# Performance work log

Hardware: AMD Instinct MI355X
Metric: run time of the kernel (lower is better)

Reference implementation:

```python
import jax, jax.numpy as jnp
import numpy as np

B, L, DIM, H, D = 2, 2048, 1024, 16, 64


def setup_inputs() -> dict:
    key = jax.random.key(0)
    ks = jax.random.split(key, 20)
    s = 1.0 / np.sqrt(DIM)
    inp = {
        "query": jax.random.normal(ks[0], (B, L, DIM), jnp.float32),
        "keys": jax.random.normal(ks[1], (B, L, DIM), jnp.float32),
        "values": jax.random.normal(ks[2], (B, L, DIM), jnp.float32),
        "focus_vector": jax.random.normal(ks[3], (B, DIM), jnp.float32),
        "temporal_weights": jax.random.normal(ks[4], (B, L), jnp.float32),
        "importance_weights": jax.random.normal(ks[5], (B, L), jnp.float32),
        # linear params, stored [in, out] for x @ W + b
        "Wq": jax.random.normal(ks[6], (DIM, H * D), jnp.float32) * s,
        "bq": jnp.zeros((H * D,), jnp.float32),
        "Wk": jax.random.normal(ks[7], (DIM, H * D), jnp.float32) * s,
        "bk": jnp.zeros((H * D,), jnp.float32),
        "Wv": jax.random.normal(ks[8], (DIM, H * D), jnp.float32) * s,
        "bv": jnp.zeros((H * D,), jnp.float32),
        "Wp": jax.random.normal(ks[9], (H * D, DIM), jnp.float32) * s,
        "bp": jnp.zeros((DIM,), jnp.float32),
        "Wt": jax.random.normal(ks[10], (DIM, 1), jnp.float32) * s,
        "bt": jnp.zeros((1,), jnp.float32),
        "Wi": jax.random.normal(ks[11], (DIM, 1), jnp.float32) * s,
        "bi": jnp.zeros((1,), jnp.float32),
    }
    return inp


def reference(query, keys, values, focus_vector, temporal_weights, importance_weights,
              Wq, bq, Wk, bk, Wv, bv, Wp, bp, Wt, bt, Wi, bi):
    b, l, _ = query.shape
    # QKV projections -> [B, H, L, D]
    q = (query @ Wq + bq).reshape(b, l, H, D).transpose(0, 2, 1, 3)
    k = (keys @ Wk + bk).reshape(b, -1, H, D).transpose(0, 2, 1, 3)
    v = (values @ Wv + bv).reshape(b, -1, H, D).transpose(0, 2, 1, 3)
    scores = jnp.einsum("bhqd,bhkd->bhqk", q, k) / np.sqrt(D).astype(np.float32)
    # gate-modulated weights over keys [B, Lk]
    temporal_scores = (keys @ Wt + bt)[..., 0]
    tw = jax.nn.softmax(temporal_scores * temporal_weights, axis=-1)
    importance_scores = (keys @ Wi + bi)[..., 0]
    iw = jax.nn.softmax(importance_scores * importance_weights, axis=-1)
    rw = jax.nn.softmax(jnp.einsum("bkd,bd->bk", keys, focus_vector), axis=-1)
    combined = (tw + iw + rw) / 3.0
    scores = scores * combined[:, None, None, :]
    weights = jax.nn.softmax(scores, axis=-1)  # dropout is identity in eval
    out = jnp.einsum("bhqk,bhkd->bhqd", weights, v)
    out = out.transpose(0, 2, 1, 3).reshape(b, l, H * D)
    out = out @ Wp + bp
    return out, weights
```

## Files before the change

kernel.cpp:

```cpp
#include <hip/hip_runtime.h>
#include <hip/hip_bf16.h>
#include <cstdint>

#define DEV static __device__ __forceinline__

typedef __attribute__((ext_vector_type(8))) short short8_;
typedef __attribute__((ext_vector_type(4))) float float4_;
typedef __attribute__((ext_vector_type(4))) float f4v;
typedef __attribute__((ext_vector_type(4))) unsigned short u16x4;
typedef unsigned short u16;

constexpr int Bb   = 2;
constexpr int Ls   = 2048;
constexpr int DIMc = 1024;
constexpr int Hh   = 16;
constexpr int Dd   = 64;
constexpr int BL   = Bb * Ls;
constexpr int HD   = Hh * Dd;

DEV u16 f2bf(float f) {
  union { float f; uint32_t u; } v; v.f = f;
  return (u16)((v.u + 0x7fffu + ((v.u >> 16) & 1u)) >> 16);
}

DEV float4_ mfma16(short8_ a, short8_ b, float4_ c) {
  return __builtin_amdgcn_mfma_f32_16x16x32_bf16(a, b, c, 0, 0, 0);
}

DEV void gload_lds16(const void* g, void* l) {
  __builtin_amdgcn_global_load_lds(
      (const __attribute__((address_space(1))) void*)g,
      (__attribute__((address_space(3))) void*)l, 16, 0, 0);
}

__global__ void k_cast3(const float* __restrict__ a, const float* __restrict__ b,
                        const float* __restrict__ c, u16* __restrict__ oa,
                        u16* __restrict__ ob, u16* __restrict__ oc) {
  int z = blockIdx.y;
  const float* s = (z == 0) ? a : (z == 1) ? b : c;
  u16* d = (z == 0) ? oa : (z == 1) ? ob : oc;
  int i = blockIdx.x * 256 + threadIdx.x;
  f4v v = ((const f4v*)s)[i];
  u16x4 o = { f2bf(v[0]), f2bf(v[1]), f2bf(v[2]), f2bf(v[3]) };
  ((u16x4*)d)[i] = o;
}

__global__ void k_trans4(const float* __restrict__ W0, const float* __restrict__ W1,
                         const float* __restrict__ W2, const float* __restrict__ W3,
                         u16* __restrict__ T0, u16* __restrict__ T1,
                         u16* __restrict__ T2, u16* __restrict__ T3) {
  __shared__ float t[64][65];
  int z = blockIdx.z;
  const float* W = (z == 0) ? W0 : (z == 1) ? W1 : (z == 2) ? W2 : W3;
  u16* WT = (z == 0) ? T0 : (z == 1) ? T1 : (z == 2) ? T2 : T3;
  int tx = threadIdx.x & 63;
  int tg = threadIdx.x >> 6;
  int n0 = blockIdx.x * 64;
  int k0 = blockIdx.y * 64;
#pragma unroll
  for (int i = 0; i < 16; ++i) {
    int r = tg * 16 + i;
    t[r][tx] = W[(size_t)(k0 + r) * HD + n0 + tx];
  }
  __syncthreads();
#pragma unroll
  for (int i = 0; i < 16; ++i) {
    int r = tg * 16 + i;
    WT[(size_t)(n0 + r) * DIMc + k0 + tx] = f2bf(t[tx][r]);
  }
}

__global__ void k_gates(const float* __restrict__ keys, const float* __restrict__ Wt,
                        const float* __restrict__ bt, const float* __restrict__ Wi,
                        const float* __restrict__ bi, const float* __restrict__ focus,
                        float* __restrict__ ts, float* __restrict__ is_, float* __restrict__ rs) {
  int wv = threadIdx.x >> 6, ln = threadIdx.x & 63;
  int row = blockIdx.x * 4 + wv;
  int b = row >> 11;
  const float* kr = keys + (size_t)row * DIMc;
  const float* fr = focus + (size_t)b * DIMc;
  float st = 0.f, si = 0.f, sr = 0.f;
  for (int j = ln; j < DIMc; j += 64) {
    float kv = kr[j];
    st += kv * Wt[j]; si += kv * Wi[j]; sr += kv * fr[j];
  }
#pragma unroll
  for (int m = 1; m < 64; m <<= 1) {
    st += __shfl_xor(st, m); si += __shfl_xor(si, m); sr += __shfl_xor(sr, m);
  }
  if (ln == 0) { ts[row] = st + bt[0]; is_[row] = si + bi[0]; rs[row] = sr; }
}

__global__ void k_combined(const float* __restrict__ ts, const float* __restrict__ is_,
                           const float* __restrict__ rs, const float* __restrict__ tw,
                           const float* __restrict__ iw, float* __restrict__ comb) {
  int b = blockIdx.x, t = threadIdx.x;
  __shared__ float red[3][4];
  float lt[8], li[8], lr[8];
  float m3[3] = {-1e30f, -1e30f, -1e30f};
#pragma unroll
  for (int i = 0; i < 8; ++i) {
    int gi = b * Ls + i * 256 + t;
    lt[i] = ts[gi] * tw[gi];
    li[i] = is_[gi] * iw[gi];
    lr[i] = rs[gi];
    m3[0] = fmaxf(m3[0], lt[i]); m3[1] = fmaxf(m3[1], li[i]); m3[2] = fmaxf(m3[2], lr[i]);
  }
#pragma unroll
  for (int q = 0; q < 3; ++q) {
    float v = m3[q];
#pragma unroll
    for (int m = 32; m; m >>= 1) v = fmaxf(v, __shfl_xor(v, m));
    if ((t & 63) == 0) red[q][t >> 6] = v;
  }
  __syncthreads();
#pragma unroll
  for (int q = 0; q < 3; ++q)
    m3[q] = fmaxf(fmaxf(red[q][0], red[q][1]), fmaxf(red[q][2], red[q][3]));
  __syncthreads();
  float s3[3] = {0.f, 0.f, 0.f};
#pragma unroll
  for (int i = 0; i < 8; ++i) {
    lt[i] = __expf(lt[i] - m3[0]); s3[0] += lt[i];
    li[i] = __expf(li[i] - m3[1]); s3[1] += li[i];
    lr[i] = __expf(lr[i] - m3[2]); s3[2] += lr[i];
  }
#pragma unroll
  for (int q = 0; q < 3; ++q) {
    float v = s3[q];
#pragma unroll
    for (int m = 32; m; m >>= 1) v += __shfl_xor(v, m);
    if ((t & 63) == 0) red[q][t >> 6] = v;
  }
  __syncthreads();
#pragma unroll
  for (int q = 0; q < 3; ++q) s3[q] = red[q][0] + red[q][1] + red[q][2] + red[q][3];
  float rt = 1.f / s3[0], ri = 1.f / s3[1], rr = 1.f / s3[2];
  const float scl = (1.f / 3.f) * 0.125f;
#pragma unroll
  for (int i = 0; i < 8; ++i) {
    int gi = b * Ls + i * 256 + t;
    comb[gi] = (lt[i] * rt + li[i] * ri + lr[i] * rr) * scl;
  }
}

__launch_bounds__(256, 2)
__global__ void k_gemm_qkv(const u16* __restrict__ qx, const u16* __restrict__ kx,
                           const u16* __restrict__ vx, const u16* __restrict__ WqT,
                           const u16* __restrict__ WkT, const u16* __restrict__ WvT,
                           const float* __restrict__ bq, const float* __restrict__ bk,
                           const float* __restrict__ bv, u16* __restrict__ q_bh,
                           u16* __restrict__ k_bh, u16* __restrict__ vT) {
  __shared__ __align__(16) u16 As[128 * 32];
  __shared__ __align__(16) u16 Bs[128 * 32];
  const int z = blockIdx.z;
  const u16* A  = (z == 0) ? qx : (z == 1) ? kx : vx;
  const u16* BT = (z == 0) ? WqT : (z == 1) ? WkT : WvT;
  const float* bias = (z == 0) ? bq : (z == 1) ? bk : bv;
  const int tid = threadIdx.x, wv = tid >> 6, ln = tid & 63;
  const int g = ln >> 4, c = ln & 15;
  const int m0 = blockIdx.x * 128, n0 = blockIdx.y * 128;
  const int wm = wv >> 1, wn = wv & 1;
  const float4_ z4 = {0.f, 0.f, 0.f, 0.f};
  float4_ acc[4][4];
#pragma unroll
  for (int i = 0; i < 4; ++i)
#pragma unroll
    for (int j = 0; j < 4; ++j) acc[i][j] = z4;
  const int lrow = ln >> 2, lcol = (ln & 3) * 8;
  for (int k0 = 0; k0 < 1024; k0 += 32) {
#pragma unroll
    for (int s = 0; s < 2; ++s) {
      int r0 = wv * 32 + s * 16;
      gload_lds16(A  + (size_t)(m0 + r0 + lrow) * 1024 + k0 + lcol, &As[r0 * 32]);
      gload_lds16(BT + (size_t)(n0 + r0 + lrow) * 1024 + k0 + lcol, &Bs[r0 * 32]);
    }
    __syncthreads();
    short8_ af[4], bfr[4];
#pragma unroll
    for (int mt = 0; mt < 4; ++mt)
      af[mt] = *(const short8_*)&As[(wm * 64 + mt * 16 + c) * 32 + g * 8];
#pragma unroll
    for (int nt = 0; nt < 4; ++nt)
      bfr[nt] = *(const short8_*)&Bs[(wn * 64 + nt * 16 + c) * 32 + g * 8];
#pragma unroll
    for (int mt = 0; mt < 4; ++mt)
#pragma unroll
      for (int nt = 0; nt < 4; ++nt)
        acc[mt][nt] = mfma16(af[mt], bfr[nt], acc[mt][nt]);
    __syncthreads();
  }
  if (z < 2) {
    u16* Q = (z == 0) ? q_bh : k_bh;
#pragma unroll
    for (int mt = 0; mt < 4; ++mt)
#pragma unroll
      for (int nt = 0; nt < 4; ++nt) {
        int n = n0 + wn * 64 + nt * 16 + c;
        float bv_ = bias[n];
        int h = n >> 6, d = n & 63;
#pragma unroll
        for (int r = 0; r < 4; ++r) {
          int m = m0 + wm * 64 + mt * 16 + g * 4 + r;
          int b = m >> 11, l = m & 2047;
          Q[((size_t)((b * Hh + h) * Ls + l)) * Dd + d] = f2bf(acc[mt][nt][r] + bv_);
        }
      }
  } else {
#pragma unroll
    for (int mt = 0; mt < 4; ++mt)
#pragma unroll
      for (int nt = 0; nt < 4; ++nt) {
        int n = n0 + wn * 64 + nt * 16 + c;
        float bv_ = bias[n];
        int h = n >> 6, d = n & 63;
        int mrow = m0 + wm * 64 + mt * 16 + g * 4;
        int b = mrow >> 11, l = mrow & 2047;
        u16x4 o = { f2bf(acc[mt][nt][0] + bv_), f2bf(acc[mt][nt][1] + bv_),
                    f2bf(acc[mt][nt][2] + bv_), f2bf(acc[mt][nt][3] + bv_) };
        *(u16x4*)&vT[((size_t)((b * Hh + h) * Dd + d)) * Ls + l] = o;
      }
  }
}

__launch_bounds__(256, 4)
__global__ void k_gemmO(const u16* __restrict__ A, const u16* __restrict__ BT,
                        const float* __restrict__ bias, float* __restrict__ O) {
  __shared__ __align__(16) u16 As[64 * 32];
  __shared__ __align__(16) u16 Bs[128 * 32];
  const int tid = threadIdx.x, wv = tid >> 6, ln = tid & 63;
  const int g = ln >> 4, c = ln & 15;
  const int m0 = blockIdx.x * 64, n0 = blockIdx.y * 128;
  const int wm = wv >> 1, wn = wv & 1;
  const float4_ z4 = {0.f, 0.f, 0.f, 0.f};
  float4_ acc[2][4];
#pragma unroll
  for (int i = 0; i < 2; ++i)
#pragma unroll
    for (int j = 0; j < 4; ++j) acc[i][j] = z4;
  const int lrow = ln >> 2, lcol = (ln & 3) * 8;
  for (int k0 = 0; k0 < 1024; k0 += 32) {
    gload_lds16(A + (size_t)(m0 + wv * 16 + lrow) * 1024 + k0 + lcol, &As[(wv * 16) * 32]);
#pragma unroll
    for (int s = 0; s < 2; ++s) {
      int r0 = wv * 32 + s * 16;
      gload_lds16(BT + (size_t)(n0 + r0 + lrow) * 1024 + k0 + lcol, &Bs[r0 * 32]);
    }
    __syncthreads();
    short8_ af[2], bfr[4];
#pragma unroll
    for (int mt = 0; mt < 2; ++mt)
      af[mt] = *(const short8_*)&As[(wm * 32 + mt * 16 + c) * 32 + g * 8];
#pragma unroll
    for (int nt = 0; nt < 4; ++nt)
      bfr[nt] = *(const short8_*)&Bs[(wn * 64 + nt * 16 + c) * 32 + g * 8];
#pragma unroll
    for (int mt = 0; mt < 2; ++mt)
#pragma unroll
      for (int nt = 0; nt < 4; ++nt)
        acc[mt][nt] = mfma16(af[mt], bfr[nt], acc[mt][nt]);
    __syncthreads();
  }
#pragma unroll
  for (int mt = 0; mt < 2; ++mt)
#pragma unroll
    for (int nt = 0; nt < 4; ++nt) {
      int n = n0 + wn * 64 + nt * 16 + c;
      float bv_ = bias[n];
#pragma unroll
      for (int r = 0; r < 4; ++r) {
        int m = m0 + wm * 32 + mt * 16 + g * 4 + r;
        O[(size_t)m * HD + n] = acc[mt][nt][r] + bv_;
      }
    }
}

__launch_bounds__(256, 4)
__global__ void k_attn3(const u16* __restrict__ q_bh, const u16* __restrict__ k_bh,
                        const u16* __restrict__ vT, const float* __restrict__ comb_g,
                        float* __restrict__ wout, u16* __restrict__ ctx) {
  __shared__ __align__(16) u16 Kt[2][64][64];
  __shared__ __align__(16) u16 Vt[2][64][64];
  __shared__ __align__(16) u16 e_w[4][16][64];

  const int bid = blockIdx.x;
  const int logical = (bid & 7) * 128 + (bid >> 3);
  const int bh = logical >> 5, qb = logical & 31;
  const int b = bh >> 4, h = bh & 15;
  const int l0 = qb * 64;
  const int w = threadIdx.x >> 6, ln = threadIdx.x & 63;
  const int g = ln >> 4, c = ln & 15;
  const int srow = ln >> 3, x8 = ln & 7;
  const float4_ z4 = {0.f, 0.f, 0.f, 0.f};

  const u16* kbh = k_bh + (size_t)bh * Ls * Dd;
  const u16* vbh = vT + (size_t)bh * Dd * Ls;
  const float* kcomb = comb_g + (size_t)b * Ls;

  const u16* qp = q_bh + ((size_t)bh * Ls + l0 + w * 16) * Dd;
  short8_ aq0 = *(const short8_*)&qp[c * Dd + g * 8];
  short8_ aq1 = *(const short8_*)&qp[c * Dd + 32 + g * 8];

  auto stageK = [&](int buf, int kb) {
#pragma unroll
    for (int i = 0; i < 2; ++i) {
      int rr = w * 16 + i * 8 + srow;
      int sc = (x8 ^ (rr & 7)) * 8;
      gload_lds16(kbh + (size_t)(kb + rr) * Dd + sc, &Kt[buf][w * 16 + i * 8][0]);
    }
  };
  auto stageV = [&](int buf, int kb) {
#pragma unroll
    for (int i = 0; i < 2; ++i) {
      int rr = w * 16 + i * 8 + srow;
      int sc = (x8 ^ (rr & 7)) * 8;
      gload_lds16(vbh + (size_t)rr * Ls + kb + sc, &Vt[buf][w * 16 + i * 8][0]);
    }
  };

  float4_ accO[4];
#pragma unroll
  for (int dt = 0; dt < 4; ++dt) accO[dt] = z4;
  float rsum4[4] = {0.f, 0.f, 0.f, 0.f};

  stageK(0, 0); stageV(0, 0);
  __syncthreads();

  int buf = 0;
  for (int t = 0; t < 32; ++t) {
    if (t < 31) { stageK(buf ^ 1, (t + 1) * 64); stageV(buf ^ 1, (t + 1) * 64); }
    const int kb = t * 64;
#pragma unroll
    for (int s = 0; s < 4; ++s) {
      int rowK = s * 16 + c;
      short8_ bk0 = *(const short8_*)&Kt[buf][rowK][((g    ) ^ (c & 7)) * 8];
      short8_ bk1 = *(const short8_*)&Kt[buf][rowK][((4 + g) ^ (c & 7)) * 8];
      float4_ st = mfma16(aq0, bk0, z4);
      st = mfma16(aq1, bk1, st);
      float cc = kcomb[kb + rowK];
      int chunk0 = s * 2 + (c >> 3), w7 = c & 7;
#pragma unroll
      for (int r = 0; r < 4; ++r) {
        float e = __expf(st[r] * cc);
        rsum4[r] += e;
        int row = g * 4 + r;
        e_w[w][row][((chunk0 ^ (row & 7)) << 3) | w7] = f2bf(e);
      }
    }
#pragma unroll
    for (int hf = 0; hf < 2; ++hf) {
      short8_ ea = *(const short8_*)&e_w[w][c][(((hf * 4 + g) ^ (c & 7)) << 3)];
#pragma unroll
      for (int dt = 0; dt < 4; ++dt) {
        short8_ bv = *(const short8_*)&Vt[buf][dt * 16 + c][((hf * 4 + g) ^ (c & 7)) * 8];
        accO[dt] = mfma16(ea, bv, accO[dt]);
      }
    }
    __syncthreads();
    buf ^= 1;
  }

#pragma unroll
  for (int m = 1; m < 16; m <<= 1)
#pragma unroll
    for (int r = 0; r < 4; ++r) rsum4[r] += __shfl_xor(rsum4[r], m);
  float invr[4];
#pragma unroll
  for (int r = 0; r < 4; ++r) invr[r] = 1.0f / rsum4[r];
  float* ivp = (float*)&e_w[w][0][0];
  if (c == 0)
#pragma unroll
    for (int r = 0; r < 4; ++r) ivp[g * 4 + r] = invr[r];

  u16* out_lds = &Vt[0][0][0] + w * 1152;
#pragma unroll
  for (int dt = 0; dt < 4; ++dt)
#pragma unroll
    for (int r = 0; r < 4; ++r)
      out_lds[(g * 4 + r) * 72 + dt * 16 + c] = f2bf(accO[dt][r] * invr[r]);
  {
    int rr2 = ln >> 2, sg = ln & 3;
    short8_ d0 = *(const short8_*)&out_lds[rr2 * 72 + sg * 16];
    short8_ d1 = *(const short8_*)&out_lds[rr2 * 72 + sg * 16 + 8];
    u16* cp = ctx + ((size_t)(b * Ls + l0 + w * 16 + rr2)) * HD + h * Dd + sg * 16;
    *(short8_*)cp = d0;
    *(short8_*)(cp + 8) = d1;
  }

  float ivq = ivp[c];
  stageK(0, 0);
  __syncthreads();
  buf = 0;
  float* wb = wout + ((size_t)bh * Ls + l0 + w * 16) * Ls;
  for (int t = 0; t < 32; ++t) {
    if (t < 31) stageK(buf ^ 1, (t + 1) * 64);
    const int kb = t * 64;
#pragma unroll
    for (int s = 0; s < 4; ++s) {
      int rowK = s * 16 + c;
      short8_ bk0 = *(const short8_*)&Kt[buf][rowK][((g    ) ^ (c & 7)) * 8];
      short8_ bk1 = *(const short8_*)&Kt[buf][rowK][((4 + g) ^ (c & 7)) * 8];
      float4_ st = mfma16(bk0, aq0, z4);
      st = mfma16(bk1, aq1, st);
      float4_ cc4 = *(const float4_*)&kcomb[kb + s * 16 + g * 4];
      float4_ o;
#pragma unroll
      for (int r = 0; r < 4; ++r) o[r] = __expf(st[r] * cc4[r]) * ivq;
      *(float4_*)&wb[(size_t)c * Ls + kb + s * 16 + g * 4] = o;
    }
    __syncthreads();
    buf ^= 1;
  }
}

extern "C" void kernel_launch(void* const* d_in, const int* in_sizes, int n_in,
                              void* d_out, int out_size, void* d_ws, size_t ws_size,
                              hipStream_t stream) {
  (void)in_sizes; (void)n_in; (void)out_size; (void)ws_size;
  const float* query = (const float*)d_in[0];
  const float* keys  = (const float*)d_in[1];
  const float* values= (const float*)d_in[2];
  const float* focus = (const float*)d_in[3];
  const float* twg   = (const float*)d_in[4];
  const float* iwg   = (const float*)d_in[5];
  const float* Wq = (const float*)d_in[6];  const float* bq = (const float*)d_in[7];
  const float* Wk = (const float*)d_in[8];  const float* bk = (const float*)d_in[9];
  const float* Wv = (const float*)d_in[10]; const float* bv = (const float*)d_in[11];
  const float* Wp = (const float*)d_in[12]; const float* bp = (const float*)d_in[13];
  const float* Wt = (const float*)d_in[14]; const float* bt = (const float*)d_in[15];
  const float* Wi = (const float*)d_in[16]; const float* bi = (const float*)d_in[17];

  char* ws = (char*)d_ws;
  size_t off = 0;
  auto alloc = [&](size_t bytes) -> char* {
    char* p = ws + off; off += (bytes + 255) & ~(size_t)255; return p;
  };
  const size_t NTOK = (size_t)BL * DIMc;
  u16* qx   = (u16*)alloc(NTOK * 2);
  u16* kx   = (u16*)alloc(NTOK * 2);
  u16* vx   = (u16*)alloc(NTOK * 2);
  u16* WqT  = (u16*)alloc((size_t)DIMc * HD * 2);
  u16* WkT  = (u16*)alloc((size_t)DIMc * HD * 2);
  u16* WvT  = (u16*)alloc((size_t)DIMc * HD * 2);
  u16* WpT  = (u16*)alloc((size_t)DIMc * HD * 2);
  u16* q_bh = (u16*)alloc(NTOK * 2);
  u16* k_bh = (u16*)alloc(NTOK * 2);
  u16* vTb  = (u16*)alloc(NTOK * 2);
  u16* ctx  = (u16*)alloc(NTOK * 2);
  float* ts   = (float*)alloc((size_t)BL * 4);
  float* is_  = (float*)alloc((size_t)BL * 4);
  float* rs   = (float*)alloc((size_t)BL * 4);
  float* comb = (float*)alloc((size_t)BL * 4);

  float* out_f = (float*)d_out;
  float* w_out = out_f + (size_t)BL * HD;

  dim3 cg(4096, 3);
  k_cast3<<<cg, 256, 0, stream>>>(query, keys, values, qx, kx, vx);
  dim3 tg(16, 16, 4);
  k_trans4<<<tg, 256, 0, stream>>>(Wq, Wk, Wv, Wp, WqT, WkT, WvT, WpT);
  k_gates<<<1024, 256, 0, stream>>>(keys, Wt, bt, Wi, bi, focus, ts, is_, rs);
  k_combined<<<2, 256, 0, stream>>>(ts, is_, rs, twg, iwg, comb);
  dim3 gq(32, 8, 3);
  k_gemm_qkv<<<gq, 256, 0, stream>>>(qx, kx, vx, WqT, WkT, WvT, bq, bk, bv,
                                     q_bh, k_bh, vTb);
  k_attn3<<<1024, 256, 0, stream>>>(q_bh, k_bh, vTb, comb, w_out, ctx);
  dim3 go(64, 8);
  k_gemmO<<<go, 256, 0, stream>>>(ctx, WpT, bp, out_f);
}
```

Measured before the change: 297.6 us.

## Merge prep kernels and overlap weight writeout with output projection

Three prep kernels (input cast, weight transpose, gate dots) become one launch dispatched by block index. The attention kernel is split: pass one computes the context and stores the per-row inverse softmax sums to global memory. A new kernel runs the output-projection GEMM blocks and the second pass that recomputes and writes the normalized attention weights side by side, so the large weight write overlaps GEMM compute. The second pass uses nontemporal stores, and the softmax numerator is repacked into 32-bit LDS writes with a transposed MFMA operand order. The cost is an extra global round trip for the inverse sums and mixed block types in one grid, which can hurt scheduling balance.

```diff
diff --git a/kernel.cpp b/kernel.cpp
--- a/kernel.cpp
+++ b/kernel.cpp
@@ -8,6 +8,7 @@
 typedef __attribute__((ext_vector_type(4))) float float4_;
 typedef __attribute__((ext_vector_type(4))) float f4v;
 typedef __attribute__((ext_vector_type(4))) unsigned short u16x4;
+typedef __attribute__((ext_vector_type(2))) uint32_t u32x2;
 typedef unsigned short u16;
 
 constexpr int Bb   = 2;
@@ -33,62 +34,63 @@
       (__attribute__((address_space(3))) void*)l, 16, 0, 0);
 }
 
-__global__ void k_cast3(const float* __restrict__ a, const float* __restrict__ b,
-                        const float* __restrict__ c, u16* __restrict__ oa,
-                        u16* __restrict__ ob, u16* __restrict__ oc) {
-  int z = blockIdx.y;
-  const float* s = (z == 0) ? a : (z == 1) ? b : c;
-  u16* d = (z == 0) ? oa : (z == 1) ? ob : oc;
-  int i = blockIdx.x * 256 + threadIdx.x;
-  f4v v = ((const f4v*)s)[i];
-  u16x4 o = { f2bf(v[0]), f2bf(v[1]), f2bf(v[2]), f2bf(v[3]) };
-  ((u16x4*)d)[i] = o;
-}
-
-__global__ void k_trans4(const float* __restrict__ W0, const float* __restrict__ W1,
-                         const float* __restrict__ W2, const float* __restrict__ W3,
-                         u16* __restrict__ T0, u16* __restrict__ T1,
-                         u16* __restrict__ T2, u16* __restrict__ T3) {
+__global__ void k_prep(const float* __restrict__ query, const float* __restrict__ keys,
+                       const float* __restrict__ values, u16* __restrict__ qx,
+                       u16* __restrict__ kx, u16* __restrict__ vx,
+                       const float* __restrict__ Wq, const float* __restrict__ Wk,
+                       const float* __restrict__ Wv, const float* __restrict__ Wp,
+                       u16* __restrict__ WqT, u16* __restrict__ WkT,
+                       u16* __restrict__ WvT, u16* __restrict__ WpT,
+                       const float* __restrict__ Wt, const float* __restrict__ bt,
+                       const float* __restrict__ Wi, const float* __restrict__ bi,
+                       const float* __restrict__ focus,
+                       float* __restrict__ ts, float* __restrict__ is_,
+                       float* __restrict__ rs) {
   __shared__ float t[64][65];
-  int z = blockIdx.z;
-  const float* W = (z == 0) ? W0 : (z == 1) ? W1 : (z == 2) ? W2 : W3;
-  u16* WT = (z == 0) ? T0 : (z == 1) ? T1 : (z == 2) ? T2 : T3;
-  int tx = threadIdx.x & 63;
-  int tg = threadIdx.x >> 6;
-  int n0 = blockIdx.x * 64;
-  int k0 = blockIdx.y * 64;
-#pragma unroll
-  for (int i = 0; i < 16; ++i) {
-    int r = tg * 16 + i;
-    t[r][tx] = W[(size_t)(k0 + r) * HD + n0 + tx];
-  }
-  __syncthreads();
-#pragma unroll
-  for (int i = 0; i < 16; ++i) {
-    int r = tg * 16 + i;
-    WT[(size_t)(n0 + r) * DIMc + k0 + tx] = f2bf(t[tx][r]);
-  }
-}
-
-__global__ void k_gates(const float* __restrict__ keys, const float* __restrict__ Wt,
-                        const float* __restrict__ bt, const float* __restrict__ Wi,
-                        const float* __restrict__ bi, const float* __restrict__ focus,
-                        float* __restrict__ ts, float* __restrict__ is_, float* __restrict__ rs) {
-  int wv = threadIdx.x >> 6, ln = threadIdx.x & 63;
-  int row = blockIdx.x * 4 + wv;
-  int b = row >> 11;
-  const float* kr = keys + (size_t)row * DIMc;
-  const float* fr = focus + (size_t)b * DIMc;
-  float st = 0.f, si = 0.f, sr = 0.f;
-  for (int j = ln; j < DIMc; j += 64) {
-    float kv = kr[j];
-    st += kv * Wt[j]; si += kv * Wi[j]; sr += kv * fr[j];
-  }
-#pragma unroll
-  for (int m = 1; m < 64; m <<= 1) {
-    st += __shfl_xor(st, m); si += __shfl_xor(si, m); sr += __shfl_xor(sr, m);
-  }
-  if (ln == 0) { ts[row] = st + bt[0]; is_[row] = si + bi[0]; rs[row] = sr; }
+  const int bid = blockIdx.x, tid = threadIdx.x;
+  if (bid < 12288) {
+    int z = bid >> 12;
+    const float* s = (z == 0) ? query : (z == 1) ? keys : values;
+    u16* d = (z == 0) ? qx : (z == 1) ? kx : vx;
+    int i = (bid & 4095) * 256 + tid;
+    f4v v = ((const f4v*)s)[i];
+    u16x4 o = { f2bf(v[0]), f2bf(v[1]), f2bf(v[2]), f2bf(v[3]) };
+    ((u16x4*)d)[i] = o;
+  } else if (bid < 13312) {
+    int r2 = bid - 12288;
+    int z = r2 >> 8, rem = r2 & 255;
+    const float* W = (z == 0) ? Wq : (z == 1) ? Wk : (z == 2) ? Wv : Wp;
+    u16* WT = (z == 0) ? WqT : (z == 1) ? WkT : (z == 2) ? WvT : WpT;
+    int n0 = (rem >> 4) * 64, k0 = (rem & 15) * 64;
+    int tx = tid & 63, tg = tid >> 6;
+#pragma unroll
+    for (int i = 0; i < 16; ++i) {
+      int r = tg * 16 + i;
+      t[r][tx] = W[(size_t)(k0 + r) * HD + n0 + tx];
+    }
+    __syncthreads();
+#pragma unroll
+    for (int i = 0; i < 16; ++i) {
+      int r = tg * 16 + i;
+      WT[(size_t)(n0 + r) * DIMc + k0 + tx] = f2bf(t[tx][r]);
+    }
+  } else {
+    int wv = tid >> 6, ln = tid & 63;
+    int row = (bid - 13312) * 4 + wv;
+    int b = row >> 11;
+    const float* kr = keys + (size_t)row * DIMc;
+    const float* fr = focus + (size_t)b * DIMc;
+    float st = 0.f, si = 0.f, sr = 0.f;
+    for (int j = ln; j < DIMc; j += 64) {
+      float kv = kr[j];
+      st += kv * Wt[j]; si += kv * Wi[j]; sr += kv * fr[j];
+    }
+#pragma unroll
+    for (int m = 1; m < 64; m <<= 1) {
+      st += __shfl_xor(st, m); si += __shfl_xor(si, m); sr += __shfl_xor(sr, m);
+    }
+    if (ln == 0) { ts[row] = st + bt[0]; is_[row] = si + bi[0]; rs[row] = sr; }
+  }
 }
 
 __global__ void k_combined(const float* __restrict__ ts, const float* __restrict__ is_,
@@ -224,64 +226,12 @@
 }
 
 __launch_bounds__(256, 4)
-__global__ void k_gemmO(const u16* __restrict__ A, const u16* __restrict__ BT,
-                        const float* __restrict__ bias, float* __restrict__ O) {
-  __shared__ __align__(16) u16 As[64 * 32];
-  __shared__ __align__(16) u16 Bs[128 * 32];
-  const int tid = threadIdx.x, wv = tid >> 6, ln = tid & 63;
-  const int g = ln >> 4, c = ln & 15;
-  const int m0 = blockIdx.x * 64, n0 = blockIdx.y * 128;
-  const int wm = wv >> 1, wn = wv & 1;
-  const float4_ z4 = {0.f, 0.f, 0.f, 0.f};
-  float4_ acc[2][4];
-#pragma unroll
-  for (int i = 0; i < 2; ++i)
-#pragma unroll
-    for (int j = 0; j < 4; ++j) acc[i][j] = z4;
-  const int lrow = ln >> 2, lcol = (ln & 3) * 8;
-  for (int k0 = 0; k0 < 1024; k0 += 32) {
-    gload_lds16(A + (size_t)(m0 + wv * 16 + lrow) * 1024 + k0 + lcol, &As[(wv * 16) * 32]);
-#pragma unroll
-    for (int s = 0; s < 2; ++s) {
-      int r0 = wv * 32 + s * 16;
-      gload_lds16(BT + (size_t)(n0 + r0 + lrow) * 1024 + k0 + lcol, &Bs[r0 * 32]);
-    }
-    __syncthreads();
-    short8_ af[2], bfr[4];
-#pragma unroll
-    for (int mt = 0; mt < 2; ++mt)
-      af[mt] = *(const short8_*)&As[(wm * 32 + mt * 16 + c) * 32 + g * 8];
-#pragma unroll
-    for (int nt = 0; nt < 4; ++nt)
-      bfr[nt] = *(const short8_*)&Bs[(wn * 64 + nt * 16 + c) * 32 + g * 8];
-#pragma unroll
-    for (int mt = 0; mt < 2; ++mt)
-#pragma unroll
-      for (int nt = 0; nt < 4; ++nt)
-        acc[mt][nt] = mfma16(af[mt], bfr[nt], acc[mt][nt]);
-    __syncthreads();
-  }
-#pragma unroll
-  for (int mt = 0; mt < 2; ++mt)
-#pragma unroll
-    for (int nt = 0; nt < 4; ++nt) {
-      int n = n0 + wn * 64 + nt * 16 + c;
-      float bv_ = bias[n];
-#pragma unroll
-      for (int r = 0; r < 4; ++r) {
-        int m = m0 + wm * 32 + mt * 16 + g * 4 + r;
-        O[(size_t)m * HD + n] = acc[mt][nt][r] + bv_;
-      }
-    }
-}
-
-__launch_bounds__(256, 4)
-__global__ void k_attn3(const u16* __restrict__ q_bh, const u16* __restrict__ k_bh,
-                        const u16* __restrict__ vT, const float* __restrict__ comb_g,
-                        float* __restrict__ wout, u16* __restrict__ ctx) {
+__global__ void k_attn_p1(const u16* __restrict__ q_bh, const u16* __restrict__ k_bh,
+                          const u16* __restrict__ vT, const float* __restrict__ comb_g,
+                          u16* __restrict__ ctx, float* __restrict__ inv_g) {
   __shared__ __align__(16) u16 Kt[2][64][64];
   __shared__ __align__(16) u16 Vt[2][64][64];
-  __shared__ __align__(16) u16 e_w[4][16][64];
+  __shared__ __align__(16) uint32_t Ew[4][16][32];
 
   const int bid = blockIdx.x;
   const int logical = (bid & 7) * 128 + (bid >> 3);
@@ -321,7 +271,7 @@
   float4_ accO[4];
 #pragma unroll
   for (int dt = 0; dt < 4; ++dt) accO[dt] = z4;
-  float rsum4[4] = {0.f, 0.f, 0.f, 0.f};
+  float rs_loc = 0.f;
 
   stageK(0, 0); stageV(0, 0);
   __syncthreads();
@@ -335,21 +285,23 @@
       int rowK = s * 16 + c;
       short8_ bk0 = *(const short8_*)&Kt[buf][rowK][((g    ) ^ (c & 7)) * 8];
       short8_ bk1 = *(const short8_*)&Kt[buf][rowK][((4 + g) ^ (c & 7)) * 8];
-      float4_ st = mfma16(aq0, bk0, z4);
-      st = mfma16(aq1, bk1, st);
-      float cc = kcomb[kb + rowK];
-      int chunk0 = s * 2 + (c >> 3), w7 = c & 7;
-#pragma unroll
-      for (int r = 0; r < 4; ++r) {
-        float e = __expf(st[r] * cc);
-        rsum4[r] += e;
-        int row = g * 4 + r;
-        e_w[w][row][((chunk0 ^ (row & 7)) << 3) | w7] = f2bf(e);
-      }
+      float4_ st = mfma16(bk0, aq0, z4);
+      st = mfma16(bk1, aq1, st);
+      float4_ cc4 = *(const float4_*)&kcomb[kb + s * 16 + g * 4];
+      float e0 = __expf(st[0] * cc4[0]);
+      float e1 = __expf(st[1] * cc4[1]);
+      float e2 = __expf(st[2] * cc4[2]);
+      float e3 = __expf(st[3] * cc4[3]);
+      rs_loc += (e0 + e1) + (e2 + e3);
+      uint32_t lo = ((uint32_t)f2bf(e1) << 16) | f2bf(e0);
+      uint32_t hi = ((uint32_t)f2bf(e3) << 16) | f2bf(e2);
+      int chunk = (s * 2 + (g >> 1)) ^ (c & 7);
+      u32x2 pk = { lo, hi };
+      *(u32x2*)&Ew[w][c][chunk * 4 + (g & 1) * 2] = pk;
     }
 #pragma unroll
     for (int hf = 0; hf < 2; ++hf) {
-      short8_ ea = *(const short8_*)&e_w[w][c][(((hf * 4 + g) ^ (c & 7)) << 3)];
+      short8_ ea = *(const short8_*)&Ew[w][c][((hf * 4 + g) ^ (c & 7)) * 4];
 #pragma unroll
       for (int dt = 0; dt < 4; ++dt) {
         short8_ bv = *(const short8_*)&Vt[buf][dt * 16 + c][((hf * 4 + g) ^ (c & 7)) * 8];
@@ -360,24 +312,20 @@
     buf ^= 1;
   }
 
-#pragma unroll
-  for (int m = 1; m < 16; m <<= 1)
-#pragma unroll
-    for (int r = 0; r < 4; ++r) rsum4[r] += __shfl_xor(rsum4[r], m);
-  float invr[4];
-#pragma unroll
-  for (int r = 0; r < 4; ++r) invr[r] = 1.0f / rsum4[r];
-  float* ivp = (float*)&e_w[w][0][0];
-  if (c == 0)
-#pragma unroll
-    for (int r = 0; r < 4; ++r) ivp[g * 4 + r] = invr[r];
+  rs_loc += __shfl_xor(rs_loc, 16);
+  rs_loc += __shfl_xor(rs_loc, 32);
+  float inv = 1.0f / rs_loc;
+  if (ln < 16) inv_g[(size_t)bh * Ls + l0 + w * 16 + ln] = inv;
+  float invrow[4];
+#pragma unroll
+  for (int r = 0; r < 4; ++r) invrow[r] = __shfl(inv, g * 4 + r);
 
   u16* out_lds = &Vt[0][0][0] + w * 1152;
 #pragma unroll
   for (int dt = 0; dt < 4; ++dt)
 #pragma unroll
     for (int r = 0; r < 4; ++r)
-      out_lds[(g * 4 + r) * 72 + dt * 16 + c] = f2bf(accO[dt][r] * invr[r]);
+      out_lds[(g * 4 + r) * 72 + dt * 16 + c] = f2bf(accO[dt][r] * invrow[r]);
   {
     int rr2 = ln >> 2, sg = ln & 3;
     short8_ d0 = *(const short8_*)&out_lds[rr2 * 72 + sg * 16];
@@ -386,30 +334,111 @@
     *(short8_*)cp = d0;
     *(short8_*)(cp + 8) = d1;
   }
-
-  float ivq = ivp[c];
-  stageK(0, 0);
-  __syncthreads();
-  buf = 0;
-  float* wb = wout + ((size_t)bh * Ls + l0 + w * 16) * Ls;
-  for (int t = 0; t < 32; ++t) {
-    if (t < 31) stageK(buf ^ 1, (t + 1) * 64);
-    const int kb = t * 64;
-#pragma unroll
-    for (int s = 0; s < 4; ++s) {
-      int rowK = s * 16 + c;
-      short8_ bk0 = *(const short8_*)&Kt[buf][rowK][((g    ) ^ (c & 7)) * 8];
-      short8_ bk1 = *(const short8_*)&Kt[buf][rowK][((4 + g) ^ (c & 7)) * 8];
-      float4_ st = mfma16(bk0, aq0, z4);
-      st = mfma16(bk1, aq1, st);
-      float4_ cc4 = *(const float4_*)&kcomb[kb + s * 16 + g * 4];
-      float4_ o;
-#pragma unroll
-      for (int r = 0; r < 4; ++r) o[r] = __expf(st[r] * cc4[r]) * ivq;
-      *(float4_*)&wb[(size_t)c * Ls + kb + s * 16 + g * 4] = o;
-    }
+}
+
+__launch_bounds__(256, 4)
+__global__ void k_p2(const u16* __restrict__ ctx, const u16* __restrict__ WpT,
+                     const float* __restrict__ bp, float* __restrict__ O,
+                     const u16* __restrict__ q_bh, const u16* __restrict__ k_bh,
+                     const float* __restrict__ comb_g, const float* __restrict__ inv_g,
+                     float* __restrict__ wout) {
+  __shared__ __align__(16) char smem[2 * 64 * 64 * 2];
+  const int tid = threadIdx.x, wv = tid >> 6, ln = tid & 63;
+  const int g = ln >> 4, c = ln & 15;
+  const float4_ z4 = {0.f, 0.f, 0.f, 0.f};
+
+  if (blockIdx.x < 512) {
+    u16* As = (u16*)smem;
+    u16* Bs = (u16*)(smem + 4096);
+    const int m0 = (int)(blockIdx.x >> 3) * 64, n0 = (int)(blockIdx.x & 7) * 128;
+    const int wm = wv >> 1, wn = wv & 1;
+    float4_ acc[2][4];
+#pragma unroll
+    for (int i = 0; i < 2; ++i)
+#pragma unroll
+      for (int j = 0; j < 4; ++j) acc[i][j] = z4;
+    const int lrow = ln >> 2, lcol = (ln & 3) * 8;
+    for (int k0 = 0; k0 < 1024; k0 += 32) {
+      gload_lds16(ctx + (size_t)(m0 + wv * 16 + lrow) * 1024 + k0 + lcol, &As[(wv * 16) * 32]);
+#pragma unroll
+      for (int s = 0; s < 2; ++s) {
+        int r0 = wv * 32 + s * 16;
+        gload_lds16(WpT + (size_t)(n0 + r0 + lrow) * 1024 + k0 + lcol, &Bs[r0 * 32]);
+      }
+      __syncthreads();
+      short8_ af[2], bfr[4];
+#pragma unroll
+      for (int mt = 0; mt < 2; ++mt)
+        af[mt] = *(const short8_*)&As[(wm * 32 + mt * 16 + c) * 32 + g * 8];
+#pragma unroll
+      for (int nt = 0; nt < 4; ++nt)
+        bfr[nt] = *(const short8_*)&Bs[(wn * 64 + nt * 16 + c) * 32 + g * 8];
+#pragma unroll
+      for (int mt = 0; mt < 2; ++mt)
+#pragma unroll
+        for (int nt = 0; nt < 4; ++nt)
+          acc[mt][nt] = mfma16(af[mt], bfr[nt], acc[mt][nt]);
+      __syncthreads();
+    }
+#pragma unroll
+    for (int mt = 0; mt < 2; ++mt)
+#pragma unroll
+      for (int nt = 0; nt < 4; ++nt) {
+        int n = n0 + wn * 64 + nt * 16 + c;
+        float bv_ = bp[n];
+#pragma unroll
+        for (int r = 0; r < 4; ++r) {
+          int m = m0 + wm * 32 + mt * 16 + g * 4 + r;
+          O[(size_t)m * HD + n] = acc[mt][nt][r] + bv_;
+        }
+      }
+  } else {
+    typedef u16 (*KtT)[64][64];
+    KtT Kt = (KtT)smem;
+    const int abid = blockIdx.x - 512;
+    const int logical = (abid & 7) * 128 + (abid >> 3);
+    const int bh = logical >> 5, qb = logical & 31;
+    const int b = bh >> 4;
+    const int l0 = qb * 64;
+    const int srow = ln >> 3, x8 = ln & 7;
+    const u16* kbh = k_bh + (size_t)bh * Ls * Dd;
+    const float* kcomb = comb_g + (size_t)b * Ls;
+    const u16* qp = q_bh + ((size_t)bh * Ls + l0 + wv * 16) * Dd;
+    short8_ aq0 = *(const short8_*)&qp[c * Dd + g * 8];
+    short8_ aq1 = *(const short8_*)&qp[c * Dd + 32 + g * 8];
+    float ivq = inv_g[(size_t)bh * Ls + l0 + wv * 16 + c];
+
+    auto stageK = [&](int buf, int kb) {
+#pragma unroll
+      for (int i = 0; i < 2; ++i) {
+        int rr = wv * 16 + i * 8 + srow;
+        int sc = (x8 ^ (rr & 7)) * 8;
+        gload_lds16(kbh + (size_t)(kb + rr) * Dd + sc, &Kt[buf][wv * 16 + i * 8][0]);
+      }
+    };
+    stageK(0, 0);
     __syncthreads();
-    buf ^= 1;
+    int buf = 0;
+    float* wb = wout + ((size_t)bh * Ls + l0 + wv * 16) * Ls;
+    for (int t = 0; t < 32; ++t) {
+      if (t < 31) stageK(buf ^ 1, (t + 1) * 64);
+      const int kb = t * 64;
+#pragma unroll
+      for (int s = 0; s < 4; ++s) {
+        int rowK = s * 16 + c;
+        short8_ bk0 = *(const short8_*)&Kt[buf][rowK][((g    ) ^ (c & 7)) * 8];
+        short8_ bk1 = *(const short8_*)&Kt[buf][rowK][((4 + g) ^ (c & 7)) * 8];
+        float4_ st = mfma16(bk0, aq0, z4);
+        st = mfma16(bk1, aq1, st);
+        float4_ cc4 = *(const float4_*)&kcomb[kb + s * 16 + g * 4];
+        float4_ o;
+#pragma unroll
+        for (int r = 0; r < 4; ++r) o[r] = __expf(st[r] * cc4[r]) * ivq;
+        __builtin_nontemporal_store(o, (float4_*)&wb[(size_t)c * Ls + kb + s * 16 + g * 4]);
+      }
+      __syncthreads();
+      buf ^= 1;
+    }
   }
 }
 
@@ -451,20 +480,19 @@
   float* is_  = (float*)alloc((size_t)BL * 4);
   float* rs   = (float*)alloc((size_t)BL * 4);
   float* comb = (float*)alloc((size_t)BL * 4);
+  float* invg = (float*)alloc((size_t)BL * 16 * 4);
 
   float* out_f = (float*)d_out;
   float* w_out = out_f + (size_t)BL * HD;
 
-  dim3 cg(4096, 3);
-  k_cast3<<<cg, 256, 0, stream>>>(query, keys, values, qx, kx, vx);
-  dim3 tg(16, 16, 4);
-  k_trans4<<<tg, 256, 0, stream>>>(Wq, Wk, Wv, Wp, WqT, WkT, WvT, WpT);
-  k_gates<<<1024, 256, 0, stream>>>(keys, Wt, bt, Wi, bi, focus, ts, is_, rs);
+  k_prep<<<14336, 256, 0, stream>>>(query, keys, values, qx, kx, vx,
+                                    Wq, Wk, Wv, Wp, WqT, WkT, WvT, WpT,
+                                    Wt, bt, Wi, bi, focus, ts, is_, rs);
   k_combined<<<2, 256, 0, stream>>>(ts, is_, rs, twg, iwg, comb);
   dim3 gq(32, 8, 3);
   k_gemm_qkv<<<gq, 256, 0, stream>>>(qx, kx, vx, WqT, WkT, WvT, bq, bk, bv,
                                      q_bh, k_bh, vTb);
-  k_attn3<<<1024, 256, 0, stream>>>(q_bh, k_bh, vTb, comb, w_out, ctx);
-  dim3 go(64, 8);
-  k_gemmO<<<go, 256, 0, stream>>>(ctx, WpT, bp, out_f);
-}
+  k_attn_p1<<<1024, 256, 0, stream>>>(q_bh, k_bh, vTb, comb, ctx, invg);
+  k_p2<<<1536, 256, 0, stream>>>(ctx, WpT, bp, out_f,
+                                 q_bh, k_bh, comb, invg, w_out);
+}
```

Measured after the change: 319.2 us. +7.3%, slower.
